# Optimization experiments

Hardware: AMD Instinct MI355X
Metric: run time of the kernel (lower is better)

The kernel has to match this reference:

```python
import jax, jax.numpy as jnp
import numpy as np

N_NODES = 1_000_000
MEM_DIM = 128
MSG_DIM = 256
N_UPD = 200_000


def setup_inputs() -> dict:
    key = jax.random.key(0)
    k0, k1, k2, k3, k4 = jax.random.split(key, 5)
    memory = jax.random.normal(k0, (N_NODES, MEM_DIM), dtype=jnp.float32)
    last_update = jnp.zeros((N_NODES,), dtype=jnp.float32)
    # 'unique' node ids: arange guarantees uniqueness and in-range values
    unique_node_ids = jnp.arange(N_UPD, dtype=jnp.int32)
    unique_messages = jax.random.normal(k1, (N_UPD, MSG_DIM), dtype=jnp.float32)
    timestamps = jax.random.uniform(k2, (N_UPD,), dtype=jnp.float32) * 1000.0
    # torch.nn.GRUCell parameters (the TGN memory_updater)
    scale = 1.0 / np.sqrt(MEM_DIM)
    W_ih = jax.random.uniform(k3, (3 * MEM_DIM, MSG_DIM), jnp.float32, -scale, scale)
    W_hh = jax.random.uniform(k4, (3 * MEM_DIM, MEM_DIM), jnp.float32, -scale, scale)
    b_ih = jnp.zeros((3 * MEM_DIM,), jnp.float32)
    b_hh = jnp.zeros((3 * MEM_DIM,), jnp.float32)
    return {
        "memory": memory,
        "last_update": last_update,
        "unique_node_ids": unique_node_ids,
        "unique_messages": unique_messages,
        "timestamps": timestamps,
        "W_ih": W_ih,
        "W_hh": W_hh,
        "b_ih": b_ih,
        "b_hh": b_hh,
    }


def _gru_cell(x, h, W_ih, W_hh, b_ih, b_hh):
    # torch.nn.GRUCell math
    gi = x @ W_ih.T + b_ih          # [U, 3H]
    gh = h @ W_hh.T + b_hh          # [U, 3H]
    i_r, i_z, i_n = jnp.split(gi, 3, axis=-1)
    h_r, h_z, h_n = jnp.split(gh, 3, axis=-1)
    r = jax.nn.sigmoid(i_r + h_r)
    z = jax.nn.sigmoid(i_z + h_z)
    n = jnp.tanh(i_n + r * h_n)
    return (1.0 - z) * n + z * h


def reference(memory, last_update, unique_node_ids, unique_messages, timestamps,
              W_ih, W_hh, b_ih, b_hh):
    # gather rows of the node memory (get_memory / updated_memory[unique_node_ids])
    h = memory[unique_node_ids]                              # [U, H]
    new_h = _gru_cell(unique_messages, h, W_ih, W_hh, b_ih, b_hh)
    # scatter updated rows back (set_memory) and update timestamps
    updated_memory = memory.at[unique_node_ids].set(new_h)
    updated_last_update = last_update.at[unique_node_ids].set(timestamps)
    return updated_memory, updated_last_update
```

## Files before the change

kernel.cpp:

```cpp
#include <hip/hip_runtime.h>
#include <hip/hip_bf16.h>
#include <stdint.h>

#define MEM_DIM 128
#define MSG_DIM 256
#define KTOT    384
#define BM      64

typedef __attribute__((ext_vector_type(8))) __bf16 bf16x8;
typedef __attribute__((ext_vector_type(4))) float  f32x4;

union B8u { uint32_t u[4]; bf16x8 v; };

__device__ __forceinline__ uint32_t cvt_pk(float lo, float hi) {
    uint32_t r;
    asm("v_cvt_pk_bf16_f32 %0, %1, %2" : "=v"(r) : "v"(lo), "v"(hi));
    return r;
}

__device__ __forceinline__ bf16x8 load_cvt8(const float* __restrict__ p) {
    f32x4 a = *(const f32x4*)p;
    f32x4 b = *(const f32x4*)(p + 4);
    B8u r;
    r.u[0] = cvt_pk(a.x, a.y);
    r.u[1] = cvt_pk(a.z, a.w);
    r.u[2] = cvt_pk(b.x, b.y);
    r.u[3] = cvt_pk(b.z, b.w);
    return r.v;
}

__device__ __forceinline__ float sigm(float x) {
    return __builtin_amdgcn_rcpf(1.0f + __expf(-x));
}
__device__ __forceinline__ float tanh_fast(float x) {
    return 1.0f - 2.0f * __builtin_amdgcn_rcpf(1.0f + __expf(2.0f * x));
}

__global__ void bm_zero_kernel(uint32_t* __restrict__ bm, int nwords) {
    int i = blockIdx.x * 256 + threadIdx.x;
    if (i < nwords) bm[i] = 0;
}
__global__ void bm_set_kernel(const int* __restrict__ ids, uint32_t* __restrict__ bm, int U) {
    int i = blockIdx.x * 256 + threadIdx.x;
    if (i < U) {
        int id = ids[i];
        atomicOr(&bm[id >> 5], 1u << (id & 31));
    }
}

__global__ void wconv_kernel(const float* __restrict__ wih,
                             const float* __restrict__ whh,
                             __hip_bfloat16* __restrict__ out) {
    int i = blockIdx.x * 256 + threadIdx.x;
    const int NIH = 3 * MEM_DIM * MSG_DIM;
    const int NHH = 3 * MEM_DIM * MEM_DIM;
    if (i < NIH)            out[i] = __float2bfloat16(wih[i]);
    else if (i < NIH + NHH) out[i] = __float2bfloat16(whh[i - NIH]);
}

__global__ void copy_skip_kernel(const f32x4* __restrict__ mem,
                                 const float* __restrict__ lu,
                                 f32x4* __restrict__ outm,
                                 float* __restrict__ outlu,
                                 const uint32_t* __restrict__ bm,
                                 int NN) {
    const int64_t n_mem_chunks = (int64_t)NN * 32;
    const int64_t total = n_mem_chunks + NN;
    const int64_t stride = (int64_t)gridDim.x * blockDim.x;
    for (int64_t i = (int64_t)blockIdx.x * blockDim.x + threadIdx.x; i < total; i += stride) {
        if (i < n_mem_chunks) {
            int row = (int)(i >> 5);
            if (!((bm[row >> 5] >> (row & 31)) & 1u)) {
                f32x4 v = __builtin_nontemporal_load(&mem[i]);
                __builtin_nontemporal_store(v, &outm[i]);
            }
        } else {
            int node = (int)(i - n_mem_chunks);
            if (!((bm[node >> 5] >> (node & 31)) & 1u))
                outlu[node] = lu[node];
        }
    }
}

__global__ void copy_all_kernel(const f32x4* __restrict__ mem,
                                const f32x4* __restrict__ lu,
                                f32x4* __restrict__ out,
                                int n_mem4, int n_tot4) {
    int stride = gridDim.x * blockDim.x;
    for (int i = blockIdx.x * blockDim.x + threadIdx.x; i < n_tot4; i += stride) {
        f32x4 v = (i < n_mem4) ? mem[i]
                               : __builtin_nontemporal_load(&lu[i - n_mem4]);
        __builtin_nontemporal_store(v, &out[i]);
    }
}

__device__ __forceinline__ int at_addr(int row, int kbyte) {
    return (row * (KTOT * 2) + kbyte) ^ ((row & 7) << 4);
}

template<bool PRE>
__global__ __launch_bounds__(512, 4)
void gru_stream_kernel(const float* __restrict__ memory,
                       const int*   __restrict__ ids,
                       const float* __restrict__ msgs,
                       const float* __restrict__ ts,
                       const float* __restrict__ Wih,
                       const float* __restrict__ Whh,
                       const float* __restrict__ bih,
                       const float* __restrict__ bhh,
                       const __hip_bfloat16* __restrict__ WihB,
                       const __hip_bfloat16* __restrict__ WhhB,
                       float* __restrict__ out_mem,
                       float* __restrict__ out_lu,
                       int U) {
    __shared__ __align__(16) char At[BM * KTOT * 2];

    const int tid  = threadIdx.x;
    const int w    = tid >> 6;
    const int lane = tid & 63;
    const int lq   = lane & 15;
    const int lk   = lane >> 4;
    const int rb   = blockIdx.x * BM;

    if (tid < BM) {
        int r = rb + tid;
        if (r < U) out_lu[ids[r]] = ts[r];
    }

    {
        int r = tid >> 3, seg = tid & 7;
        int rA = rb + r; if (rA >= U) rA = U - 1;
        const float* xp = msgs + (size_t)rA * MSG_DIM + seg * 32;
        #pragma unroll
        for (int i = 0; i < 4; ++i)
            *(bf16x8*)(At + at_addr(r, seg * 64 + i * 16)) = load_cvt8(xp + i * 8);
    }
    {
        int r = tid >> 3, u = tid & 7;
        int rA = rb + r; if (rA >= U) rA = U - 1;
        const float* hp = memory + (size_t)ids[rA] * MEM_DIM + u * 16;
        *(bf16x8*)(At + at_addr(r, 512 + u * 32))      = load_cvt8(hp);
        *(bf16x8*)(At + at_addr(r, 512 + u * 32 + 16)) = load_cvt8(hp + 8);
    }

    const int c = w * 16 + lq;
    const float br  = bih[c] + bhh[c];
    const float bz  = bih[MEM_DIM + c] + bhh[MEM_DIM + c];
    const float bin = bih[2 * MEM_DIM + c];
    const float bhn = bhh[2 * MEM_DIM + c];

    const __hip_bfloat16* wih_l = WihB + c * MSG_DIM + lk * 8;
    const __hip_bfloat16* whh_l = WhhB + c * MEM_DIM + lk * 8;
    const float* wih_f = Wih + c * MSG_DIM + lk * 8;
    const float* whh_f = Whh + c * MEM_DIM + lk * 8;

    const f32x4 z4 = {0.f, 0.f, 0.f, 0.f};
    f32x4 acc[4][4];
    #pragma unroll
    for (int m = 0; m < 4; ++m)
        #pragma unroll
        for (int q = 0; q < 4; ++q) acc[m][q] = z4;

    __syncthreads();

    #pragma unroll 1
    for (int ks = 0; ks < 8; ++ks) {
        bf16x8 bv0, bv1, bv2;
        if (PRE) {
            bv0 = *(const bf16x8*)(wih_l + 0 * 128 * MSG_DIM + ks * 32);
            bv1 = *(const bf16x8*)(wih_l + 1 * 128 * MSG_DIM + ks * 32);
            bv2 = *(const bf16x8*)(wih_l + 2 * 128 * MSG_DIM + ks * 32);
        } else {
            bv0 = load_cvt8(wih_f + 0 * 128 * MSG_DIM + ks * 32);
            bv1 = load_cvt8(wih_f + 1 * 128 * MSG_DIM + ks * 32);
            bv2 = load_cvt8(wih_f + 2 * 128 * MSG_DIM + ks * 32);
        }
        bf16x8 af[4];
        #pragma unroll
        for (int m = 0; m < 4; ++m)
            af[m] = *(const bf16x8*)(At + at_addr(m * 16 + lq, ks * 64 + lk * 16));
        #pragma unroll
        for (int m = 0; m < 4; ++m)
            acc[m][0] = __builtin_amdgcn_mfma_f32_16x16x32_bf16(af[m], bv0, acc[m][0], 0, 0, 0);
        #pragma unroll
        for (int m = 0; m < 4; ++m)
            acc[m][1] = __builtin_amdgcn_mfma_f32_16x16x32_bf16(af[m], bv1, acc[m][1], 0, 0, 0);
        #pragma unroll
        for (int m = 0; m < 4; ++m)
            acc[m][2] = __builtin_amdgcn_mfma_f32_16x16x32_bf16(af[m], bv2, acc[m][2], 0, 0, 0);
    }
    #pragma unroll 1
    for (int ks = 0; ks < 4; ++ks) {
        bf16x8 bv0, bv1, bv2;
        if (PRE) {
            bv0 = *(const bf16x8*)(whh_l + 0 * 128 * MEM_DIM + ks * 32);
            bv1 = *(const bf16x8*)(whh_l + 1 * 128 * MEM_DIM + ks * 32);
            bv2 = *(const bf16x8*)(whh_l + 2 * 128 * MEM_DIM + ks * 32);
        } else {
            bv0 = load_cvt8(whh_f + 0 * 128 * MEM_DIM + ks * 32);
            bv1 = load_cvt8(whh_f + 1 * 128 * MEM_DIM + ks * 32);
            bv2 = load_cvt8(whh_f + 2 * 128 * MEM_DIM + ks * 32);
        }
        bf16x8 af[4];
        #pragma unroll
        for (int m = 0; m < 4; ++m)
            af[m] = *(const bf16x8*)(At + at_addr(m * 16 + lq, 512 + ks * 64 + lk * 16));
        #pragma unroll
        for (int m = 0; m < 4; ++m)
            acc[m][0] = __builtin_amdgcn_mfma_f32_16x16x32_bf16(af[m], bv0, acc[m][0], 0, 0, 0);
        #pragma unroll
        for (int m = 0; m < 4; ++m)
            acc[m][1] = __builtin_amdgcn_mfma_f32_16x16x32_bf16(af[m], bv1, acc[m][1], 0, 0, 0);
        #pragma unroll
        for (int m = 0; m < 4; ++m)
            acc[m][3] = __builtin_amdgcn_mfma_f32_16x16x32_bf16(af[m], bv2, acc[m][3], 0, 0, 0);
    }

    #pragma unroll
    for (int m = 0; m < 4; ++m) {
        #pragma unroll
        for (int j = 0; j < 4; ++j) {
            int row = m * 16 + lk * 4 + j;
            int r = rb + row;
            if (r < U) {
                int id = ids[r];
                float hold = __bfloat162float(
                    *(const __hip_bfloat16*)(At + at_addr(row, 512 + c * 2)));
                float rg = sigm(acc[m][0][j] + br);
                float zg = sigm(acc[m][1][j] + bz);
                float ng = tanh_fast(acc[m][2][j] + bin + rg * (acc[m][3][j] + bhn));
                out_mem[(size_t)id * MEM_DIM + c] = (1.0f - zg) * ng + zg * hold;
            }
        }
    }
}

extern "C" void kernel_launch(void* const* d_in, const int* in_sizes, int n_in,
                              void* d_out, int out_size, void* d_ws, size_t ws_size,
                              hipStream_t stream) {
    const float* memory      = (const float*)d_in[0];
    const float* last_update = (const float*)d_in[1];
    const int*   ids         = (const int*)  d_in[2];
    const float* msgs        = (const float*)d_in[3];
    const float* ts          = (const float*)d_in[4];
    const float* Wih         = (const float*)d_in[5];
    const float* Whh         = (const float*)d_in[6];
    const float* bih         = (const float*)d_in[7];
    const float* bhh         = (const float*)d_in[8];

    const int NN = in_sizes[1];
    const int U  = in_sizes[2];

    float* out_mem = (float*)d_out;
    float* out_lu  = out_mem + (size_t)NN * MEM_DIM;

    const int NIH = 3 * MEM_DIM * MSG_DIM;
    const int NHH = 3 * MEM_DIM * MEM_DIM;
    const size_t WBYTES  = (size_t)(NIH + NHH) * sizeof(__hip_bfloat16);
    const size_t BM_OFF  = (WBYTES + 255) & ~(size_t)255;
    const int    BMWORDS = (NN + 31) / 32;
    const int    nblocks = (U + BM - 1) / BM;

    if (ws_size >= BM_OFF + (size_t)BMWORDS * 4) {
        __hip_bfloat16* wb = (__hip_bfloat16*)d_ws;
        uint32_t* bm = (uint32_t*)((char*)d_ws + BM_OFF);

        wconv_kernel<<<(NIH + NHH + 255) / 256, 256, 0, stream>>>(Wih, Whh, wb);
        bm_zero_kernel<<<(BMWORDS + 255) / 256, 256, 0, stream>>>(bm, BMWORDS);
        bm_set_kernel<<<(U + 255) / 256, 256, 0, stream>>>(ids, bm, U);

        gru_stream_kernel<true><<<nblocks, 512, 0, stream>>>(
            memory, ids, msgs, ts, Wih, Whh, bih, bhh,
            wb, wb + NIH, out_mem, out_lu, U);

        copy_skip_kernel<<<8192, 256, 0, stream>>>((const f32x4*)memory, last_update,
                                                   (f32x4*)out_mem, out_lu, bm, NN);
    } else {
        int n_mem4 = NN * MEM_DIM / 4;
        int n_tot4 = n_mem4 + NN / 4;
        copy_all_kernel<<<8192, 256, 0, stream>>>((const f32x4*)memory,
                                                  (const f32x4*)last_update,
                                                  (f32x4*)d_out, n_mem4, n_tot4);
        gru_stream_kernel<false><<<nblocks, 512, 0, stream>>>(
            memory, ids, msgs, ts, Wih, Whh, bih, bhh,
            nullptr, nullptr, out_mem, out_lu, U);
    }
}
```

Measured before the change: 353.4 us.

## Pre-pack GRU weights in MFMA fragment order and fuse init kernels

Weight conversion now writes bf16 weights in a per-wave, per-lane fragment layout, so each lane's B-operand load is a contiguous 16-byte chunk and a wave reads 1 KB contiguously. The bitmap zeroing is merged into the same init kernel, removing one launch. The epilogue reloads the old hidden state in fp32 from global memory into registers before the MMA loop, instead of reading the bf16 copy from LDS, which also makes the blend exact. Output rows are written with nontemporal stores. The extra per-thread gathers of 16 hidden values add memory traffic and register pressure, and some dead leftover code remains.

```diff
diff --git a/kernel.cpp b/kernel.cpp
--- a/kernel.cpp
+++ b/kernel.cpp
@@ -36,9 +36,32 @@
     return 1.0f - 2.0f * __builtin_amdgcn_rcpf(1.0f + __expf(2.0f * x));
 }
 
-__global__ void bm_zero_kernel(uint32_t* __restrict__ bm, int nwords) {
-    int i = blockIdx.x * 256 + threadIdx.x;
-    if (i < nwords) bm[i] = 0;
+__global__ void init_kernel(const float* __restrict__ wih,
+                            const float* __restrict__ whh,
+                            __hip_bfloat16* __restrict__ wp,
+                            uint32_t* __restrict__ bm, int bmwords) {
+    int u = blockIdx.x * 256 + threadIdx.x;
+    const int XU = 8 * 3 * 8 * 64;
+    const int HU = 4 * 3 * 8 * 64;
+    if (u < XU) {
+        int group = u >> 6, lane = u & 63;
+        int ks = group / 24, g = (group % 24) >> 3, w = group & 7;
+        int lq = lane & 15, lk = lane >> 4;
+        const float* src = wih + (size_t)(g * 128 + w * 16 + lq) * MSG_DIM + ks * 32 + lk * 8;
+        __hip_bfloat16* dst = wp + (size_t)u * 8;
+        #pragma unroll
+        for (int i = 0; i < 8; ++i) dst[i] = __float2bfloat16(src[i]);
+    } else if (u < XU + HU) {
+        int v = u - XU;
+        int group = v >> 6, lane = v & 63;
+        int ks = group / 24, g = (group % 24) >> 3, w = group & 7;
+        int lq = lane & 15, lk = lane >> 4;
+        const float* src = whh + (size_t)(g * 128 + w * 16 + lq) * MEM_DIM + ks * 32 + lk * 8;
+        __hip_bfloat16* dst = wp + (size_t)(XU + v) * 8;
+        #pragma unroll
+        for (int i = 0; i < 8; ++i) dst[i] = __float2bfloat16(src[i]);
+    }
+    if (u < bmwords) bm[u] = 0;
 }
 __global__ void bm_set_kernel(const int* __restrict__ ids, uint32_t* __restrict__ bm, int U) {
     int i = blockIdx.x * 256 + threadIdx.x;
@@ -46,16 +69,6 @@
         int id = ids[i];
         atomicOr(&bm[id >> 5], 1u << (id & 31));
     }
-}
-
-__global__ void wconv_kernel(const float* __restrict__ wih,
-                             const float* __restrict__ whh,
-                             __hip_bfloat16* __restrict__ out) {
-    int i = blockIdx.x * 256 + threadIdx.x;
-    const int NIH = 3 * MEM_DIM * MSG_DIM;
-    const int NHH = 3 * MEM_DIM * MEM_DIM;
-    if (i < NIH)            out[i] = __float2bfloat16(wih[i]);
-    else if (i < NIH + NHH) out[i] = __float2bfloat16(whh[i - NIH]);
 }
 
 __global__ void copy_skip_kernel(const f32x4* __restrict__ mem,
@@ -108,8 +121,7 @@
                        const float* __restrict__ Whh,
                        const float* __restrict__ bih,
                        const float* __restrict__ bhh,
-                       const __hip_bfloat16* __restrict__ WihB,
-                       const __hip_bfloat16* __restrict__ WhhB,
+                       const __hip_bfloat16* __restrict__ WP,
                        float* __restrict__ out_mem,
                        float* __restrict__ out_lu,
                        int U) {
@@ -149,8 +161,8 @@
     const float bin = bih[2 * MEM_DIM + c];
     const float bhn = bhh[2 * MEM_DIM + c];
 
-    const __hip_bfloat16* wih_l = WihB + c * MSG_DIM + lk * 8;
-    const __hip_bfloat16* whh_l = WhhB + c * MEM_DIM + lk * 8;
+    const __hip_bfloat16* wpx = WP + (size_t)w * 512 + lane * 8;
+    const __hip_bfloat16* wph = WP + (size_t)(8 * 3 * 8 * 64) * 8 + (size_t)w * 512 + lane * 8;
     const float* wih_f = Wih + c * MSG_DIM + lk * 8;
     const float* whh_f = Whh + c * MEM_DIM + lk * 8;
 
@@ -163,13 +175,32 @@
 
     __syncthreads();
 
+    int   oid[4];
+    float hv[4];
+    #pragma unroll
+    for (int j = 0; j < 4; ++j) {
+        int r = rb + (lk << 2) + j;
+        (void)r;
+    }
+    int   oidm[4][4];
+    float hvm[4][4];
+    #pragma unroll
+    for (int m = 0; m < 4; ++m)
+        #pragma unroll
+        for (int j = 0; j < 4; ++j) {
+            int r = rb + m * 16 + lk * 4 + j;
+            oidm[m][j] = ids[(r < U) ? r : (U - 1)];
+            hvm[m][j]  = memory[(size_t)oidm[m][j] * MEM_DIM + c];
+        }
+
     #pragma unroll 1
     for (int ks = 0; ks < 8; ++ks) {
         bf16x8 bv0, bv1, bv2;
         if (PRE) {
-            bv0 = *(const bf16x8*)(wih_l + 0 * 128 * MSG_DIM + ks * 32);
-            bv1 = *(const bf16x8*)(wih_l + 1 * 128 * MSG_DIM + ks * 32);
-            bv2 = *(const bf16x8*)(wih_l + 2 * 128 * MSG_DIM + ks * 32);
+            const __hip_bfloat16* p = wpx + (size_t)ks * 24 * 512;
+            bv0 = *(const bf16x8*)(p);
+            bv1 = *(const bf16x8*)(p + 8 * 512);
+            bv2 = *(const bf16x8*)(p + 16 * 512);
         } else {
             bv0 = load_cvt8(wih_f + 0 * 128 * MSG_DIM + ks * 32);
             bv1 = load_cvt8(wih_f + 1 * 128 * MSG_DIM + ks * 32);
@@ -193,9 +224,10 @@
     for (int ks = 0; ks < 4; ++ks) {
         bf16x8 bv0, bv1, bv2;
         if (PRE) {
-            bv0 = *(const bf16x8*)(whh_l + 0 * 128 * MEM_DIM + ks * 32);
-            bv1 = *(const bf16x8*)(whh_l + 1 * 128 * MEM_DIM + ks * 32);
-            bv2 = *(const bf16x8*)(whh_l + 2 * 128 * MEM_DIM + ks * 32);
+            const __hip_bfloat16* p = wph + (size_t)ks * 24 * 512;
+            bv0 = *(const bf16x8*)(p);
+            bv1 = *(const bf16x8*)(p + 8 * 512);
+            bv2 = *(const bf16x8*)(p + 16 * 512);
         } else {
             bv0 = load_cvt8(whh_f + 0 * 128 * MEM_DIM + ks * 32);
             bv1 = load_cvt8(whh_f + 1 * 128 * MEM_DIM + ks * 32);
@@ -220,16 +252,14 @@
     for (int m = 0; m < 4; ++m) {
         #pragma unroll
         for (int j = 0; j < 4; ++j) {
-            int row = m * 16 + lk * 4 + j;
-            int r = rb + row;
+            int r = rb + m * 16 + lk * 4 + j;
             if (r < U) {
-                int id = ids[r];
-                float hold = __bfloat162float(
-                    *(const __hip_bfloat16*)(At + at_addr(row, 512 + c * 2)));
                 float rg = sigm(acc[m][0][j] + br);
                 float zg = sigm(acc[m][1][j] + bz);
                 float ng = tanh_fast(acc[m][2][j] + bin + rg * (acc[m][3][j] + bhn));
-                out_mem[(size_t)id * MEM_DIM + c] = (1.0f - zg) * ng + zg * hold;
+                __builtin_nontemporal_store(
+                    (1.0f - zg) * ng + zg * hvm[m][j],
+                    &out_mem[(size_t)oidm[m][j] * MEM_DIM + c]);
             }
         }
     }
@@ -262,16 +292,16 @@
     const int    nblocks = (U + BM - 1) / BM;
 
     if (ws_size >= BM_OFF + (size_t)BMWORDS * 4) {
-        __hip_bfloat16* wb = (__hip_bfloat16*)d_ws;
+        __hip_bfloat16* wp = (__hip_bfloat16*)d_ws;
         uint32_t* bm = (uint32_t*)((char*)d_ws + BM_OFF);
 
-        wconv_kernel<<<(NIH + NHH + 255) / 256, 256, 0, stream>>>(Wih, Whh, wb);
-        bm_zero_kernel<<<(BMWORDS + 255) / 256, 256, 0, stream>>>(bm, BMWORDS);
+        int initn = ((NIH + NHH) / 8 > BMWORDS) ? (NIH + NHH) / 8 : BMWORDS;
+        init_kernel<<<(initn + 255) / 256, 256, 0, stream>>>(Wih, Whh, wp, bm, BMWORDS);
         bm_set_kernel<<<(U + 255) / 256, 256, 0, stream>>>(ids, bm, U);
 
         gru_stream_kernel<true><<<nblocks, 512, 0, stream>>>(
             memory, ids, msgs, ts, Wih, Whh, bih, bhh,
-            wb, wb + NIH, out_mem, out_lu, U);
+            wp, out_mem, out_lu, U);
 
         copy_skip_kernel<<<8192, 256, 0, stream>>>((const f32x4*)memory, last_update,
                                                    (f32x4*)out_mem, out_lu, bm, NN);
@@ -283,6 +313,6 @@
                                                   (f32x4*)d_out, n_mem4, n_tot4);
         gru_stream_kernel<false><<<nblocks, 512, 0, stream>>>(
             memory, ids, msgs, ts, Wih, Whh, bih, bhh,
-            nullptr, nullptr, out_mem, out_lu, U);
-    }
-}
+            nullptr, out_mem, out_lu, U);
+    }
+}
```

New measurement: 400.9 us. 13.4% more time.

## Make GRU kernel persistent with double-buffered LDS prefetch of next tile

Applied to the files above, without the earlier changes.

Changes the GRU kernel from one block per 64-row tile to a persistent grid of 256 blocks that loop over tiles. Each block loads the next tile's messages and gathered memory rows into registers while it computes the current tile, then writes them into a second LDS slab. The weight-conversion and bitmap-zero kernels are merged into one launch to save a launch. The cost is doubled LDS, more registers, lower occupancy (launch bounds 2), and extra barriers per tile.

```diff
diff --git a/kernel.cpp b/kernel.cpp
--- a/kernel.cpp
+++ b/kernel.cpp
@@ -6,6 +6,7 @@
 #define MSG_DIM 256
 #define KTOT    384
 #define BM      64
+#define SLAB    (BM * KTOT * 2)
 
 typedef __attribute__((ext_vector_type(8))) __bf16 bf16x8;
 typedef __attribute__((ext_vector_type(4))) float  f32x4;
@@ -18,9 +19,7 @@
     return r;
 }
 
-__device__ __forceinline__ bf16x8 load_cvt8(const float* __restrict__ p) {
-    f32x4 a = *(const f32x4*)p;
-    f32x4 b = *(const f32x4*)(p + 4);
+__device__ __forceinline__ bf16x8 pack8(f32x4 a, f32x4 b) {
     B8u r;
     r.u[0] = cvt_pk(a.x, a.y);
     r.u[1] = cvt_pk(a.z, a.w);
@@ -29,6 +28,10 @@
     return r.v;
 }
 
+__device__ __forceinline__ bf16x8 load_cvt8(const float* __restrict__ p) {
+    return pack8(*(const f32x4*)p, *(const f32x4*)(p + 4));
+}
+
 __device__ __forceinline__ float sigm(float x) {
     return __builtin_amdgcn_rcpf(1.0f + __expf(-x));
 }
@@ -36,9 +39,16 @@
     return 1.0f - 2.0f * __builtin_amdgcn_rcpf(1.0f + __expf(2.0f * x));
 }
 
-__global__ void bm_zero_kernel(uint32_t* __restrict__ bm, int nwords) {
+__global__ void init_kernel(const float* __restrict__ wih,
+                            const float* __restrict__ whh,
+                            __hip_bfloat16* __restrict__ wb,
+                            uint32_t* __restrict__ bm, int bmwords) {
     int i = blockIdx.x * 256 + threadIdx.x;
-    if (i < nwords) bm[i] = 0;
+    const int NIH = 3 * MEM_DIM * MSG_DIM;
+    const int NHH = 3 * MEM_DIM * MEM_DIM;
+    if (i < NIH)            wb[i] = __float2bfloat16(wih[i]);
+    else if (i < NIH + NHH) wb[i] = __float2bfloat16(whh[i - NIH]);
+    if (i < bmwords) bm[i] = 0;
 }
 __global__ void bm_set_kernel(const int* __restrict__ ids, uint32_t* __restrict__ bm, int U) {
     int i = blockIdx.x * 256 + threadIdx.x;
@@ -46,16 +56,6 @@
         int id = ids[i];
         atomicOr(&bm[id >> 5], 1u << (id & 31));
     }
-}
-
-__global__ void wconv_kernel(const float* __restrict__ wih,
-                             const float* __restrict__ whh,
-                             __hip_bfloat16* __restrict__ out) {
-    int i = blockIdx.x * 256 + threadIdx.x;
-    const int NIH = 3 * MEM_DIM * MSG_DIM;
-    const int NHH = 3 * MEM_DIM * MEM_DIM;
-    if (i < NIH)            out[i] = __float2bfloat16(wih[i]);
-    else if (i < NIH + NHH) out[i] = __float2bfloat16(whh[i - NIH]);
 }
 
 __global__ void copy_skip_kernel(const f32x4* __restrict__ mem,
@@ -99,49 +99,29 @@
 }
 
 template<bool PRE>
-__global__ __launch_bounds__(512, 4)
-void gru_stream_kernel(const float* __restrict__ memory,
-                       const int*   __restrict__ ids,
-                       const float* __restrict__ msgs,
-                       const float* __restrict__ ts,
-                       const float* __restrict__ Wih,
-                       const float* __restrict__ Whh,
-                       const float* __restrict__ bih,
-                       const float* __restrict__ bhh,
-                       const __hip_bfloat16* __restrict__ WihB,
-                       const __hip_bfloat16* __restrict__ WhhB,
-                       float* __restrict__ out_mem,
-                       float* __restrict__ out_lu,
-                       int U) {
-    __shared__ __align__(16) char At[BM * KTOT * 2];
+__global__ __launch_bounds__(512, 2)
+void gru_pipe_kernel(const float* __restrict__ memory,
+                     const int*   __restrict__ ids,
+                     const float* __restrict__ msgs,
+                     const float* __restrict__ ts,
+                     const float* __restrict__ Wih,
+                     const float* __restrict__ Whh,
+                     const float* __restrict__ bih,
+                     const float* __restrict__ bhh,
+                     const __hip_bfloat16* __restrict__ WihB,
+                     const __hip_bfloat16* __restrict__ WhhB,
+                     float* __restrict__ out_mem,
+                     float* __restrict__ out_lu,
+                     int U, int ntiles) {
+    __shared__ __align__(16) char At[2][SLAB];
 
     const int tid  = threadIdx.x;
     const int w    = tid >> 6;
     const int lane = tid & 63;
     const int lq   = lane & 15;
     const int lk   = lane >> 4;
-    const int rb   = blockIdx.x * BM;
-
-    if (tid < BM) {
-        int r = rb + tid;
-        if (r < U) out_lu[ids[r]] = ts[r];
-    }
-
-    {
-        int r = tid >> 3, seg = tid & 7;
-        int rA = rb + r; if (rA >= U) rA = U - 1;
-        const float* xp = msgs + (size_t)rA * MSG_DIM + seg * 32;
-        #pragma unroll
-        for (int i = 0; i < 4; ++i)
-            *(bf16x8*)(At + at_addr(r, seg * 64 + i * 16)) = load_cvt8(xp + i * 8);
-    }
-    {
-        int r = tid >> 3, u = tid & 7;
-        int rA = rb + r; if (rA >= U) rA = U - 1;
-        const float* hp = memory + (size_t)ids[rA] * MEM_DIM + u * 16;
-        *(bf16x8*)(At + at_addr(r, 512 + u * 32))      = load_cvt8(hp);
-        *(bf16x8*)(At + at_addr(r, 512 + u * 32 + 16)) = load_cvt8(hp + 8);
-    }
+
+    const int xr = tid >> 3, xseg = tid & 7;
 
     const int c = w * 16 + lq;
     const float br  = bih[c] + bhh[c];
@@ -154,84 +134,126 @@
     const float* wih_f = Wih + c * MSG_DIM + lk * 8;
     const float* whh_f = Whh + c * MEM_DIM + lk * 8;
 
-    const f32x4 z4 = {0.f, 0.f, 0.f, 0.f};
-    f32x4 acc[4][4];
-    #pragma unroll
-    for (int m = 0; m < 4; ++m)
-        #pragma unroll
-        for (int q = 0; q < 4; ++q) acc[m][q] = z4;
-
+    f32x4 xa[8];
+    f32x4 ha[4];
+
+    auto ISSUE = [&](int t) {
+        int rA = t * BM + xr; if (rA >= U) rA = U - 1;
+        const float* xp = msgs + (size_t)rA * MSG_DIM + xseg * 32;
+        #pragma unroll
+        for (int i = 0; i < 8; ++i) xa[i] = *(const f32x4*)(xp + i * 4);
+        const float* hp = memory + (size_t)ids[rA] * MEM_DIM + xseg * 16;
+        #pragma unroll
+        for (int i = 0; i < 4; ++i) ha[i] = *(const f32x4*)(hp + i * 4);
+        if (tid < BM) {
+            int r = t * BM + tid;
+            if (r < U) out_lu[ids[r]] = ts[r];
+        }
+    };
+    auto WRITE = [&](char* base) {
+        #pragma unroll
+        for (int i = 0; i < 4; ++i)
+            *(bf16x8*)(base + at_addr(xr, xseg * 64 + i * 16)) =
+                pack8(xa[2 * i], xa[2 * i + 1]);
+        *(bf16x8*)(base + at_addr(xr, 512 + xseg * 32))      = pack8(ha[0], ha[1]);
+        *(bf16x8*)(base + at_addr(xr, 512 + xseg * 32 + 16)) = pack8(ha[2], ha[3]);
+    };
+
+    int t = blockIdx.x;
+    if (t >= ntiles) return;
+
+    ISSUE(t);
+    WRITE(At[0]);
     __syncthreads();
 
-    #pragma unroll 1
-    for (int ks = 0; ks < 8; ++ks) {
-        bf16x8 bv0, bv1, bv2;
-        if (PRE) {
-            bv0 = *(const bf16x8*)(wih_l + 0 * 128 * MSG_DIM + ks * 32);
-            bv1 = *(const bf16x8*)(wih_l + 1 * 128 * MSG_DIM + ks * 32);
-            bv2 = *(const bf16x8*)(wih_l + 2 * 128 * MSG_DIM + ks * 32);
-        } else {
-            bv0 = load_cvt8(wih_f + 0 * 128 * MSG_DIM + ks * 32);
-            bv1 = load_cvt8(wih_f + 1 * 128 * MSG_DIM + ks * 32);
-            bv2 = load_cvt8(wih_f + 2 * 128 * MSG_DIM + ks * 32);
-        }
-        bf16x8 af[4];
+    int cur = 0;
+    for (; t < ntiles; t += gridDim.x, cur ^= 1) {
+        const int tn = t + gridDim.x;
+        const bool hasnext = (tn < ntiles);
+        if (hasnext) ISSUE(tn);
+
+        char* base = At[cur];
+        const f32x4 z4 = {0.f, 0.f, 0.f, 0.f};
+        f32x4 acc[4][4];
         #pragma unroll
         for (int m = 0; m < 4; ++m)
-            af[m] = *(const bf16x8*)(At + at_addr(m * 16 + lq, ks * 64 + lk * 16));
-        #pragma unroll
-        for (int m = 0; m < 4; ++m)
-            acc[m][0] = __builtin_amdgcn_mfma_f32_16x16x32_bf16(af[m], bv0, acc[m][0], 0, 0, 0);
-        #pragma unroll
-        for (int m = 0; m < 4; ++m)
-            acc[m][1] = __builtin_amdgcn_mfma_f32_16x16x32_bf16(af[m], bv1, acc[m][1], 0, 0, 0);
-        #pragma unroll
-        for (int m = 0; m < 4; ++m)
-            acc[m][2] = __builtin_amdgcn_mfma_f32_16x16x32_bf16(af[m], bv2, acc[m][2], 0, 0, 0);
-    }
-    #pragma unroll 1
-    for (int ks = 0; ks < 4; ++ks) {
-        bf16x8 bv0, bv1, bv2;
-        if (PRE) {
-            bv0 = *(const bf16x8*)(whh_l + 0 * 128 * MEM_DIM + ks * 32);
-            bv1 = *(const bf16x8*)(whh_l + 1 * 128 * MEM_DIM + ks * 32);
-            bv2 = *(const bf16x8*)(whh_l + 2 * 128 * MEM_DIM + ks * 32);
-        } else {
-            bv0 = load_cvt8(whh_f + 0 * 128 * MEM_DIM + ks * 32);
-            bv1 = load_cvt8(whh_f + 1 * 128 * MEM_DIM + ks * 32);
-            bv2 = load_cvt8(whh_f + 2 * 128 * MEM_DIM + ks * 32);
-        }
-        bf16x8 af[4];
-        #pragma unroll
-        for (int m = 0; m < 4; ++m)
-            af[m] = *(const bf16x8*)(At + at_addr(m * 16 + lq, 512 + ks * 64 + lk * 16));
-        #pragma unroll
-        for (int m = 0; m < 4; ++m)
-            acc[m][0] = __builtin_amdgcn_mfma_f32_16x16x32_bf16(af[m], bv0, acc[m][0], 0, 0, 0);
-        #pragma unroll
-        for (int m = 0; m < 4; ++m)
-            acc[m][1] = __builtin_amdgcn_mfma_f32_16x16x32_bf16(af[m], bv1, acc[m][1], 0, 0, 0);
-        #pragma unroll
-        for (int m = 0; m < 4; ++m)
-            acc[m][3] = __builtin_amdgcn_mfma_f32_16x16x32_bf16(af[m], bv2, acc[m][3], 0, 0, 0);
-    }
-
-    #pragma unroll
-    for (int m = 0; m < 4; ++m) {
-        #pragma unroll
-        for (int j = 0; j < 4; ++j) {
-            int row = m * 16 + lk * 4 + j;
-            int r = rb + row;
-            if (r < U) {
-                int id = ids[r];
-                float hold = __bfloat162float(
-                    *(const __hip_bfloat16*)(At + at_addr(row, 512 + c * 2)));
-                float rg = sigm(acc[m][0][j] + br);
-                float zg = sigm(acc[m][1][j] + bz);
-                float ng = tanh_fast(acc[m][2][j] + bin + rg * (acc[m][3][j] + bhn));
-                out_mem[(size_t)id * MEM_DIM + c] = (1.0f - zg) * ng + zg * hold;
+            #pragma unroll
+            for (int q = 0; q < 4; ++q) acc[m][q] = z4;
+
+        #pragma unroll
+        for (int ks = 0; ks < 8; ++ks) {
+            bf16x8 bv0, bv1, bv2;
+            if (PRE) {
+                bv0 = *(const bf16x8*)(wih_l + 0 * 128 * MSG_DIM + ks * 32);
+                bv1 = *(const bf16x8*)(wih_l + 1 * 128 * MSG_DIM + ks * 32);
+                bv2 = *(const bf16x8*)(wih_l + 2 * 128 * MSG_DIM + ks * 32);
+            } else {
+                bv0 = load_cvt8(wih_f + 0 * 128 * MSG_DIM + ks * 32);
+                bv1 = load_cvt8(wih_f + 1 * 128 * MSG_DIM + ks * 32);
+                bv2 = load_cvt8(wih_f + 2 * 128 * MSG_DIM + ks * 32);
             }
-        }
+            bf16x8 af[4];
+            #pragma unroll
+            for (int m = 0; m < 4; ++m)
+                af[m] = *(const bf16x8*)(base + at_addr(m * 16 + lq, ks * 64 + lk * 16));
+            #pragma unroll
+            for (int m = 0; m < 4; ++m)
+                acc[m][0] = __builtin_amdgcn_mfma_f32_16x16x32_bf16(af[m], bv0, acc[m][0], 0, 0, 0);
+            #pragma unroll
+            for (int m = 0; m < 4; ++m)
+                acc[m][1] = __builtin_amdgcn_mfma_f32_16x16x32_bf16(af[m], bv1, acc[m][1], 0, 0, 0);
+            #pragma unroll
+            for (int m = 0; m < 4; ++m)
+                acc[m][2] = __builtin_amdgcn_mfma_f32_16x16x32_bf16(af[m], bv2, acc[m][2], 0, 0, 0);
+        }
+        #pragma unroll
+        for (int ks = 0; ks < 4; ++ks) {
+            bf16x8 bv0, bv1, bv2;
+            if (PRE) {
+                bv0 = *(const bf16x8*)(whh_l + 0 * 128 * MEM_DIM + ks * 32);
+                bv1 = *(const bf16x8*)(whh_l + 1 * 128 * MEM_DIM + ks * 32);
+                bv2 = *(const bf16x8*)(whh_l + 2 * 128 * MEM_DIM + ks * 32);
+            } else {
+                bv0 = load_cvt8(whh_f + 0 * 128 * MEM_DIM + ks * 32);
+                bv1 = load_cvt8(whh_f + 1 * 128 * MEM_DIM + ks * 32);
+                bv2 = load_cvt8(whh_f + 2 * 128 * MEM_DIM + ks * 32);
+            }
+            bf16x8 af[4];
+            #pragma unroll
+            for (int m = 0; m < 4; ++m)
+                af[m] = *(const bf16x8*)(base + at_addr(m * 16 + lq, 512 + ks * 64 + lk * 16));
+            #pragma unroll
+            for (int m = 0; m < 4; ++m)
+                acc[m][0] = __builtin_amdgcn_mfma_f32_16x16x32_bf16(af[m], bv0, acc[m][0], 0, 0, 0);
+            #pragma unroll
+            for (int m = 0; m < 4; ++m)
+                acc[m][1] = __builtin_amdgcn_mfma_f32_16x16x32_bf16(af[m], bv1, acc[m][1], 0, 0, 0);
+            #pragma unroll
+            for (int m = 0; m < 4; ++m)
+                acc[m][3] = __builtin_amdgcn_mfma_f32_16x16x32_bf16(af[m], bv2, acc[m][3], 0, 0, 0);
+        }
+
+        #pragma unroll
+        for (int m = 0; m < 4; ++m) {
+            #pragma unroll
+            for (int j = 0; j < 4; ++j) {
+                int row = m * 16 + lk * 4 + j;
+                int r = t * BM + row;
+                if (r < U) {
+                    int id = ids[r];
+                    float hold = __bfloat162float(
+                        *(const __hip_bfloat16*)(base + at_addr(row, 512 + c * 2)));
+                    float rg = sigm(acc[m][0][j] + br);
+                    float zg = sigm(acc[m][1][j] + bz);
+                    float ng = tanh_fast(acc[m][2][j] + bin + rg * (acc[m][3][j] + bhn));
+                    out_mem[(size_t)id * MEM_DIM + c] = (1.0f - zg) * ng + zg * hold;
+                }
+            }
+        }
+
+        __syncthreads();
+        if (hasnext) WRITE(At[cur ^ 1]);
+        __syncthreads();
     }
 }
 
@@ -259,19 +281,19 @@
     const size_t WBYTES  = (size_t)(NIH + NHH) * sizeof(__hip_bfloat16);
     const size_t BM_OFF  = (WBYTES + 255) & ~(size_t)255;
     const int    BMWORDS = (NN + 31) / 32;
-    const int    nblocks = (U + BM - 1) / BM;
+    const int    ntiles  = (U + BM - 1) / BM;
 
     if (ws_size >= BM_OFF + (size_t)BMWORDS * 4) {
         __hip_bfloat16* wb = (__hip_bfloat16*)d_ws;
         uint32_t* bm = (uint32_t*)((char*)d_ws + BM_OFF);
 
-        wconv_kernel<<<(NIH + NHH + 255) / 256, 256, 0, stream>>>(Wih, Whh, wb);
-        bm_zero_kernel<<<(BMWORDS + 255) / 256, 256, 0, stream>>>(bm, BMWORDS);
+        int initn = (NIH + NHH > BMWORDS) ? (NIH + NHH) : BMWORDS;
+        init_kernel<<<(initn + 255) / 256, 256, 0, stream>>>(Wih, Whh, wb, bm, BMWORDS);
         bm_set_kernel<<<(U + 255) / 256, 256, 0, stream>>>(ids, bm, U);
 
-        gru_stream_kernel<true><<<nblocks, 512, 0, stream>>>(
+        gru_pipe_kernel<true><<<256, 512, 0, stream>>>(
             memory, ids, msgs, ts, Wih, Whh, bih, bhh,
-            wb, wb + NIH, out_mem, out_lu, U);
+            wb, wb + NIH, out_mem, out_lu, U, ntiles);
 
         copy_skip_kernel<<<8192, 256, 0, stream>>>((const f32x4*)memory, last_update,
                                                    (f32x4*)out_mem, out_lu, bm, NN);
@@ -281,8 +303,8 @@
         copy_all_kernel<<<8192, 256, 0, stream>>>((const f32x4*)memory,
                                                   (const f32x4*)last_update,
                                                   (f32x4*)d_out, n_mem4, n_tot4);
-        gru_stream_kernel<false><<<nblocks, 512, 0, stream>>>(
+        gru_pipe_kernel<false><<<256, 512, 0, stream>>>(
             memory, ids, msgs, ts, Wih, Whh, bih, bhh,
-            nullptr, nullptr, out_mem, out_lu, U);
-    }
-}
+            nullptr, nullptr, out_mem, out_lu, U, ntiles);
+    }
+}
```

Result: slower. 581.8 us (+64.6%).

## Fuse GRU tiles and masked copy into one interleaved kernel launch

Applied to the files above, without the earlier changes.

Merges the GRU compute kernel and the bitmap-masked memory copy into a single launch. Blocks are assigned proportionally to either a GRU tile or a copy role, so compute-heavy MFMA blocks and bandwidth-heavy copy blocks run concurrently and no kernel boundary sits between them. The weight conversion and bitmap zeroing kernels are also merged into one init kernel to save a launch. The risk is that copy blocks with 512 threads and a fixed count of 2048 may get a different effective grid shape than before, and LDS allocation for copy blocks limits their occupancy.

```diff
diff --git a/kernel.cpp b/kernel.cpp
--- a/kernel.cpp
+++ b/kernel.cpp
@@ -6,6 +6,7 @@
 #define MSG_DIM 256
 #define KTOT    384
 #define BM      64
+#define NCOPY   2048
 
 typedef __attribute__((ext_vector_type(8))) __bf16 bf16x8;
 typedef __attribute__((ext_vector_type(4))) float  f32x4;
@@ -36,49 +37,22 @@
     return 1.0f - 2.0f * __builtin_amdgcn_rcpf(1.0f + __expf(2.0f * x));
 }
 
-__global__ void bm_zero_kernel(uint32_t* __restrict__ bm, int nwords) {
+__global__ void init_kernel(const float* __restrict__ wih,
+                            const float* __restrict__ whh,
+                            __hip_bfloat16* __restrict__ wb,
+                            uint32_t* __restrict__ bm, int bmwords) {
     int i = blockIdx.x * 256 + threadIdx.x;
-    if (i < nwords) bm[i] = 0;
+    const int NIH = 3 * MEM_DIM * MSG_DIM;
+    const int NHH = 3 * MEM_DIM * MEM_DIM;
+    if (i < NIH)            wb[i] = __float2bfloat16(wih[i]);
+    else if (i < NIH + NHH) wb[i] = __float2bfloat16(whh[i - NIH]);
+    if (i < bmwords) bm[i] = 0;
 }
 __global__ void bm_set_kernel(const int* __restrict__ ids, uint32_t* __restrict__ bm, int U) {
     int i = blockIdx.x * 256 + threadIdx.x;
     if (i < U) {
         int id = ids[i];
         atomicOr(&bm[id >> 5], 1u << (id & 31));
-    }
-}
-
-__global__ void wconv_kernel(const float* __restrict__ wih,
-                             const float* __restrict__ whh,
-                             __hip_bfloat16* __restrict__ out) {
-    int i = blockIdx.x * 256 + threadIdx.x;
-    const int NIH = 3 * MEM_DIM * MSG_DIM;
-    const int NHH = 3 * MEM_DIM * MEM_DIM;
-    if (i < NIH)            out[i] = __float2bfloat16(wih[i]);
-    else if (i < NIH + NHH) out[i] = __float2bfloat16(whh[i - NIH]);
-}
-
-__global__ void copy_skip_kernel(const f32x4* __restrict__ mem,
-                                 const float* __restrict__ lu,
-                                 f32x4* __restrict__ outm,
-                                 float* __restrict__ outlu,
-                                 const uint32_t* __restrict__ bm,
-                                 int NN) {
-    const int64_t n_mem_chunks = (int64_t)NN * 32;
-    const int64_t total = n_mem_chunks + NN;
-    const int64_t stride = (int64_t)gridDim.x * blockDim.x;
-    for (int64_t i = (int64_t)blockIdx.x * blockDim.x + threadIdx.x; i < total; i += stride) {
-        if (i < n_mem_chunks) {
-            int row = (int)(i >> 5);
-            if (!((bm[row >> 5] >> (row & 31)) & 1u)) {
-                f32x4 v = __builtin_nontemporal_load(&mem[i]);
-                __builtin_nontemporal_store(v, &outm[i]);
-            }
-        } else {
-            int node = (int)(i - n_mem_chunks);
-            if (!((bm[node >> 5] >> (node & 31)) & 1u))
-                outlu[node] = lu[node];
-        }
     }
 }
 
@@ -100,136 +74,167 @@
 
 template<bool PRE>
 __global__ __launch_bounds__(512, 4)
-void gru_stream_kernel(const float* __restrict__ memory,
-                       const int*   __restrict__ ids,
-                       const float* __restrict__ msgs,
-                       const float* __restrict__ ts,
-                       const float* __restrict__ Wih,
-                       const float* __restrict__ Whh,
-                       const float* __restrict__ bih,
-                       const float* __restrict__ bhh,
-                       const __hip_bfloat16* __restrict__ WihB,
-                       const __hip_bfloat16* __restrict__ WhhB,
-                       float* __restrict__ out_mem,
-                       float* __restrict__ out_lu,
-                       int U) {
+void gru_mix_kernel(const float* __restrict__ memory,
+                    const int*   __restrict__ ids,
+                    const float* __restrict__ msgs,
+                    const float* __restrict__ ts,
+                    const float* __restrict__ Wih,
+                    const float* __restrict__ Whh,
+                    const float* __restrict__ bih,
+                    const float* __restrict__ bhh,
+                    const __hip_bfloat16* __restrict__ WihB,
+                    const __hip_bfloat16* __restrict__ WhhB,
+                    const uint32_t* __restrict__ bm,
+                    const float* __restrict__ last_update,
+                    float* __restrict__ out_mem,
+                    float* __restrict__ out_lu,
+                    int U, int ntiles, int total, int NN) {
     __shared__ __align__(16) char At[BM * KTOT * 2];
 
-    const int tid  = threadIdx.x;
-    const int w    = tid >> 6;
-    const int lane = tid & 63;
-    const int lq   = lane & 15;
-    const int lk   = lane >> 4;
-    const int rb   = blockIdx.x * BM;
-
-    if (tid < BM) {
-        int r = rb + tid;
-        if (r < U) out_lu[ids[r]] = ts[r];
-    }
-
-    {
-        int r = tid >> 3, seg = tid & 7;
-        int rA = rb + r; if (rA >= U) rA = U - 1;
-        const float* xp = msgs + (size_t)rA * MSG_DIM + seg * 32;
-        #pragma unroll
-        for (int i = 0; i < 4; ++i)
-            *(bf16x8*)(At + at_addr(r, seg * 64 + i * 16)) = load_cvt8(xp + i * 8);
-    }
-    {
-        int r = tid >> 3, u = tid & 7;
-        int rA = rb + r; if (rA >= U) rA = U - 1;
-        const float* hp = memory + (size_t)ids[rA] * MEM_DIM + u * 16;
-        *(bf16x8*)(At + at_addr(r, 512 + u * 32))      = load_cvt8(hp);
-        *(bf16x8*)(At + at_addr(r, 512 + u * 32 + 16)) = load_cvt8(hp + 8);
-    }
-
-    const int c = w * 16 + lq;
-    const float br  = bih[c] + bhh[c];
-    const float bz  = bih[MEM_DIM + c] + bhh[MEM_DIM + c];
-    const float bin = bih[2 * MEM_DIM + c];
-    const float bhn = bhh[2 * MEM_DIM + c];
-
-    const __hip_bfloat16* wih_l = WihB + c * MSG_DIM + lk * 8;
-    const __hip_bfloat16* whh_l = WhhB + c * MEM_DIM + lk * 8;
-    const float* wih_f = Wih + c * MSG_DIM + lk * 8;
-    const float* whh_f = Whh + c * MEM_DIM + lk * 8;
-
-    const f32x4 z4 = {0.f, 0.f, 0.f, 0.f};
-    f32x4 acc[4][4];
-    #pragma unroll
-    for (int m = 0; m < 4; ++m)
-        #pragma unroll
-        for (int q = 0; q < 4; ++q) acc[m][q] = z4;
-
-    __syncthreads();
-
-    #pragma unroll 1
-    for (int ks = 0; ks < 8; ++ks) {
-        bf16x8 bv0, bv1, bv2;
-        if (PRE) {
-            bv0 = *(const bf16x8*)(wih_l + 0 * 128 * MSG_DIM + ks * 32);
-            bv1 = *(const bf16x8*)(wih_l + 1 * 128 * MSG_DIM + ks * 32);
-            bv2 = *(const bf16x8*)(wih_l + 2 * 128 * MSG_DIM + ks * 32);
-        } else {
-            bv0 = load_cvt8(wih_f + 0 * 128 * MSG_DIM + ks * 32);
-            bv1 = load_cvt8(wih_f + 1 * 128 * MSG_DIM + ks * 32);
-            bv2 = load_cvt8(wih_f + 2 * 128 * MSG_DIM + ks * 32);
-        }
-        bf16x8 af[4];
+    const int bid = blockIdx.x;
+    const int tid = threadIdx.x;
+
+    const int64_t g0 = ((int64_t)bid * ntiles) / total;
+    const int64_t g1 = ((int64_t)(bid + 1) * ntiles) / total;
+
+    if (g1 > g0) {
+        const int t    = (int)g0;
+        const int w    = tid >> 6;
+        const int lane = tid & 63;
+        const int lq   = lane & 15;
+        const int lk   = lane >> 4;
+        const int rb   = t * BM;
+
+        if (tid < BM) {
+            int r = rb + tid;
+            if (r < U) out_lu[ids[r]] = ts[r];
+        }
+
+        {
+            int r = tid >> 3, seg = tid & 7;
+            int rA = rb + r; if (rA >= U) rA = U - 1;
+            const float* xp = msgs + (size_t)rA * MSG_DIM + seg * 32;
+            #pragma unroll
+            for (int i = 0; i < 4; ++i)
+                *(bf16x8*)(At + at_addr(r, seg * 64 + i * 16)) = load_cvt8(xp + i * 8);
+        }
+        {
+            int r = tid >> 3, u = tid & 7;
+            int rA = rb + r; if (rA >= U) rA = U - 1;
+            const float* hp = memory + (size_t)ids[rA] * MEM_DIM + u * 16;
+            *(bf16x8*)(At + at_addr(r, 512 + u * 32))      = load_cvt8(hp);
+            *(bf16x8*)(At + at_addr(r, 512 + u * 32 + 16)) = load_cvt8(hp + 8);
+        }
+
+        const int c = w * 16 + lq;
+        const float br  = bih[c] + bhh[c];
+        const float bz  = bih[MEM_DIM + c] + bhh[MEM_DIM + c];
+        const float bin = bih[2 * MEM_DIM + c];
+        const float bhn = bhh[2 * MEM_DIM + c];
+
+        const __hip_bfloat16* wih_l = WihB + c * MSG_DIM + lk * 8;
+        const __hip_bfloat16* whh_l = WhhB + c * MEM_DIM + lk * 8;
+        const float* wih_f = Wih + c * MSG_DIM + lk * 8;
+        const float* whh_f = Whh + c * MEM_DIM + lk * 8;
+
+        const f32x4 z4 = {0.f, 0.f, 0.f, 0.f};
+        f32x4 acc[4][4];
         #pragma unroll
         for (int m = 0; m < 4; ++m)
-            af[m] = *(const bf16x8*)(At + at_addr(m * 16 + lq, ks * 64 + lk * 16));
+            #pragma unroll
+            for (int q = 0; q < 4; ++q) acc[m][q] = z4;
+
+        __syncthreads();
+
+        #pragma unroll 1
+        for (int ks = 0; ks < 8; ++ks) {
+            bf16x8 bv0, bv1, bv2;
+            if (PRE) {
+                bv0 = *(const bf16x8*)(wih_l + 0 * 128 * MSG_DIM + ks * 32);
+                bv1 = *(const bf16x8*)(wih_l + 1 * 128 * MSG_DIM + ks * 32);
+                bv2 = *(const bf16x8*)(wih_l + 2 * 128 * MSG_DIM + ks * 32);
+            } else {
+                bv0 = load_cvt8(wih_f + 0 * 128 * MSG_DIM + ks * 32);
+                bv1 = load_cvt8(wih_f + 1 * 128 * MSG_DIM + ks * 32);
+                bv2 = load_cvt8(wih_f + 2 * 128 * MSG_DIM + ks * 32);
+            }
+            bf16x8 af[4];
+            #pragma unroll
+            for (int m = 0; m < 4; ++m)
+                af[m] = *(const bf16x8*)(At + at_addr(m * 16 + lq, ks * 64 + lk * 16));
+            #pragma unroll
+            for (int m = 0; m < 4; ++m)
+                acc[m][0] = __builtin_amdgcn_mfma_f32_16x16x32_bf16(af[m], bv0, acc[m][0], 0, 0, 0);
+            #pragma unroll
+            for (int m = 0; m < 4; ++m)
+                acc[m][1] = __builtin_amdgcn_mfma_f32_16x16x32_bf16(af[m], bv1, acc[m][1], 0, 0, 0);
+            #pragma unroll
+            for (int m = 0; m < 4; ++m)
+                acc[m][2] = __builtin_amdgcn_mfma_f32_16x16x32_bf16(af[m], bv2, acc[m][2], 0, 0, 0);
+        }
+        #pragma unroll 1
+        for (int ks = 0; ks < 4; ++ks) {
+            bf16x8 bv0, bv1, bv2;
+            if (PRE) {
+                bv0 = *(const bf16x8*)(whh_l + 0 * 128 * MEM_DIM + ks * 32);
+                bv1 = *(const bf16x8*)(whh_l + 1 * 128 * MEM_DIM + ks * 32);
+                bv2 = *(const bf16x8*)(whh_l + 2 * 128 * MEM_DIM + ks * 32);
+            } else {
+                bv0 = load_cvt8(whh_f + 0 * 128 * MEM_DIM + ks * 32);
+                bv1 = load_cvt8(whh_f + 1 * 128 * MEM_DIM + ks * 32);
+                bv2 = load_cvt8(whh_f + 2 * 128 * MEM_DIM + ks * 32);
+            }
+            bf16x8 af[4];
+            #pragma unroll
+            for (int m = 0; m < 4; ++m)
+                af[m] = *(const bf16x8*)(At + at_addr(m * 16 + lq, 512 + ks * 64 + lk * 16));
+            #pragma unroll
+            for (int m = 0; m < 4; ++m)
+                acc[m][0] = __builtin_amdgcn_mfma_f32_16x16x32_bf16(af[m], bv0, acc[m][0], 0, 0, 0);
+            #pragma unroll
+            for (int m = 0; m < 4; ++m)
+                acc[m][1] = __builtin_amdgcn_mfma_f32_16x16x32_bf16(af[m], bv1, acc[m][1], 0, 0, 0);
+            #pragma unroll
+            for (int m = 0; m < 4; ++m)
+                acc[m][3] = __builtin_amdgcn_mfma_f32_16x16x32_bf16(af[m], bv2, acc[m][3], 0, 0, 0);
+        }
+
         #pragma unroll
-        for (int m = 0; m < 4; ++m)
-            acc[m][0] = __builtin_amdgcn_mfma_f32_16x16x32_bf16(af[m], bv0, acc[m][0], 0, 0, 0);
-        #pragma unroll
-        for (int m = 0; m < 4; ++m)
-            acc[m][1] = __builtin_amdgcn_mfma_f32_16x16x32_bf16(af[m], bv1, acc[m][1], 0, 0, 0);
-        #pragma unroll
-        for (int m = 0; m < 4; ++m)
-            acc[m][2] = __builtin_amdgcn_mfma_f32_16x16x32_bf16(af[m], bv2, acc[m][2], 0, 0, 0);
-    }
-    #pragma unroll 1
-    for (int ks = 0; ks < 4; ++ks) {
-        bf16x8 bv0, bv1, bv2;
-        if (PRE) {
-            bv0 = *(const bf16x8*)(whh_l + 0 * 128 * MEM_DIM + ks * 32);
-            bv1 = *(const bf16x8*)(whh_l + 1 * 128 * MEM_DIM + ks * 32);
-            bv2 = *(const bf16x8*)(whh_l + 2 * 128 * MEM_DIM + ks * 32);
-        } else {
-            bv0 = load_cvt8(whh_f + 0 * 128 * MEM_DIM + ks * 32);
-            bv1 = load_cvt8(whh_f + 1 * 128 * MEM_DIM + ks * 32);
-            bv2 = load_cvt8(whh_f + 2 * 128 * MEM_DIM + ks * 32);
-        }
-        bf16x8 af[4];
-        #pragma unroll
-        for (int m = 0; m < 4; ++m)
-            af[m] = *(const bf16x8*)(At + at_addr(m * 16 + lq, 512 + ks * 64 + lk * 16));
-        #pragma unroll
-        for (int m = 0; m < 4; ++m)
-            acc[m][0] = __builtin_amdgcn_mfma_f32_16x16x32_bf16(af[m], bv0, acc[m][0], 0, 0, 0);
-        #pragma unroll
-        for (int m = 0; m < 4; ++m)
-            acc[m][1] = __builtin_amdgcn_mfma_f32_16x16x32_bf16(af[m], bv1, acc[m][1], 0, 0, 0);
-        #pragma unroll
-        for (int m = 0; m < 4; ++m)
-            acc[m][3] = __builtin_amdgcn_mfma_f32_16x16x32_bf16(af[m], bv2, acc[m][3], 0, 0, 0);
-    }
-
-    #pragma unroll
-    for (int m = 0; m < 4; ++m) {
-        #pragma unroll
-        for (int j = 0; j < 4; ++j) {
-            int row = m * 16 + lk * 4 + j;
-            int r = rb + row;
-            if (r < U) {
-                int id = ids[r];
-                float hold = __bfloat162float(
-                    *(const __hip_bfloat16*)(At + at_addr(row, 512 + c * 2)));
-                float rg = sigm(acc[m][0][j] + br);
-                float zg = sigm(acc[m][1][j] + bz);
-                float ng = tanh_fast(acc[m][2][j] + bin + rg * (acc[m][3][j] + bhn));
-                out_mem[(size_t)id * MEM_DIM + c] = (1.0f - zg) * ng + zg * hold;
+        for (int m = 0; m < 4; ++m) {
+            #pragma unroll
+            for (int j = 0; j < 4; ++j) {
+                int row = m * 16 + lk * 4 + j;
+                int r = rb + row;
+                if (r < U) {
+                    int id = ids[r];
+                    float hold = __bfloat162float(
+                        *(const __hip_bfloat16*)(At + at_addr(row, 512 + c * 2)));
+                    float rg = sigm(acc[m][0][j] + br);
+                    float zg = sigm(acc[m][1][j] + bz);
+                    float ng = tanh_fast(acc[m][2][j] + bin + rg * (acc[m][3][j] + bhn));
+                    out_mem[(size_t)id * MEM_DIM + c] = (1.0f - zg) * ng + zg * hold;
+                }
+            }
+        }
+    } else {
+        const int64_t ncopy = total - ntiles;
+        const int64_t ord   = bid - g0;
+        const int64_t n_mem_chunks = (int64_t)NN * 32;
+        const int64_t tot = n_mem_chunks + NN;
+        const int64_t stride = ncopy * 512;
+        const f32x4* memv = (const f32x4*)memory;
+        f32x4* outv = (f32x4*)out_mem;
+        for (int64_t i = ord * 512 + tid; i < tot; i += stride) {
+            if (i < n_mem_chunks) {
+                int row = (int)(i >> 5);
+                if (!((bm[row >> 5] >> (row & 31)) & 1u)) {
+                    f32x4 v = __builtin_nontemporal_load(&memv[i]);
+                    __builtin_nontemporal_store(v, &outv[i]);
+                }
+            } else {
+                int node = (int)(i - n_mem_chunks);
+                if (!((bm[node >> 5] >> (node & 31)) & 1u))
+                    out_lu[node] = last_update[node];
             }
         }
     }
@@ -259,30 +264,29 @@
     const size_t WBYTES  = (size_t)(NIH + NHH) * sizeof(__hip_bfloat16);
     const size_t BM_OFF  = (WBYTES + 255) & ~(size_t)255;
     const int    BMWORDS = (NN + 31) / 32;
-    const int    nblocks = (U + BM - 1) / BM;
+    const int    ntiles  = (U + BM - 1) / BM;
+    const int    total   = ntiles + NCOPY;
 
     if (ws_size >= BM_OFF + (size_t)BMWORDS * 4) {
         __hip_bfloat16* wb = (__hip_bfloat16*)d_ws;
         uint32_t* bm = (uint32_t*)((char*)d_ws + BM_OFF);
 
-        wconv_kernel<<<(NIH + NHH + 255) / 256, 256, 0, stream>>>(Wih, Whh, wb);
-        bm_zero_kernel<<<(BMWORDS + 255) / 256, 256, 0, stream>>>(bm, BMWORDS);
+        int initn = (NIH + NHH > BMWORDS) ? (NIH + NHH) : BMWORDS;
+        init_kernel<<<(initn + 255) / 256, 256, 0, stream>>>(Wih, Whh, wb, bm, BMWORDS);
         bm_set_kernel<<<(U + 255) / 256, 256, 0, stream>>>(ids, bm, U);
 
-        gru_stream_kernel<true><<<nblocks, 512, 0, stream>>>(
+        gru_mix_kernel<true><<<total, 512, 0, stream>>>(
             memory, ids, msgs, ts, Wih, Whh, bih, bhh,
-            wb, wb + NIH, out_mem, out_lu, U);
-
-        copy_skip_kernel<<<8192, 256, 0, stream>>>((const f32x4*)memory, last_update,
-                                                   (f32x4*)out_mem, out_lu, bm, NN);
+            wb, wb + NIH, bm, last_update, out_mem, out_lu, U, ntiles, total, NN);
     } else {
         int n_mem4 = NN * MEM_DIM / 4;
         int n_tot4 = n_mem4 + NN / 4;
         copy_all_kernel<<<8192, 256, 0, stream>>>((const f32x4*)memory,
                                                   (const f32x4*)last_update,
                                                   (f32x4*)d_out, n_mem4, n_tot4);
-        gru_stream_kernel<false><<<nblocks, 512, 0, stream>>>(
+        gru_mix_kernel<false><<<ntiles, 512, 0, stream>>>(
             memory, ids, msgs, ts, Wih, Whh, bih, bhh,
-            nullptr, nullptr, out_mem, out_lu, U);
-    }
-}
+            nullptr, nullptr, nullptr, last_update, out_mem, out_lu,
+            U, ntiles, ntiles, NN);
+    }
+}
```

Measured after the change: 403.8 us. 14.3% more time.
